# Optimization experiments

Hardware: AMD Instinct MI355X
Metric: run time of the kernel (lower is better)

## Reference

```python
import jax, jax.numpy as jnp
import numpy as np

D_MODEL = 1024
D_FF = 2 * D_MODEL
N_EXPERTS = 8
TOP_K = 2
SCAT_SCALE = 0.1


def setup_inputs() -> dict:
    key = jax.random.key(0)
    ks = jax.random.split(key, 8)
    s_in = 1.0 / np.sqrt(D_MODEL)
    s_ff = 1.0 / np.sqrt(D_FF)
    return {
        "x": jax.random.normal(ks[0], (4, 2048, D_MODEL), dtype=jnp.float32),
        "Wg": jax.random.uniform(ks[1], (D_MODEL, N_EXPERTS), minval=-s_in, maxval=s_in),
        "bg": jax.random.uniform(ks[2], (N_EXPERTS,), minval=-s_in, maxval=s_in),
        "W1": jax.random.uniform(ks[3], (N_EXPERTS, D_MODEL, D_FF), minval=-s_in, maxval=s_in),
        "b1": jax.random.uniform(ks[4], (N_EXPERTS, D_FF), minval=-s_in, maxval=s_in),
        "W2": jax.random.uniform(ks[5], (N_EXPERTS, D_FF, D_MODEL), minval=-s_ff, maxval=s_ff),
        "b2": jax.random.uniform(ks[6], (N_EXPERTS, D_MODEL), minval=-s_ff, maxval=s_ff),
    }


def reference(x, Wg, bg, W1, b1, W2, b2):
    B, N, D = x.shape
    T = B * N
    xf = x.reshape(T, D)

    # gating logits + norm-based modulation (scattering_scale branch)
    logits = xf @ Wg + bg  # [T, E]
    tnorm = jnp.linalg.norm(xf, axis=-1, keepdims=True)  # [T, 1]
    norm_scaled = (tnorm - tnorm.mean()) / (jnp.std(tnorm, ddof=1) + 1e-6)
    logits = logits + SCAT_SCALE * norm_scaled

    # top-k routing
    topv, topi = jax.lax.top_k(logits, TOP_K)  # [T, K]
    gates_k = jax.nn.softmax(topv, axis=-1)  # [T, K]
    routing_entropy = -(gates_k * jnp.log(jnp.clip(gates_k, 1e-8, None))).sum(-1).mean()

    # dense per-token expert-weight matrix (zeros for non-selected experts)
    E = W1.shape[0]
    gates = jnp.zeros((T, E), dtype=gates_k.dtype).at[
        jnp.arange(T)[:, None], topi
    ].add(gates_k)  # [T, E]

    # all-expert MLP (dense equivalent of sparse dispatch; weight 0 -> no contribution)
    h = jax.nn.relu(jnp.einsum("td,edf->etf", xf, W1) + b1[:, None, :])  # [E, T, F]
    y = jnp.einsum("etf,efd->etd", h, W2) + b2[:, None, :]  # [E, T, D]
    out = jnp.einsum("etd,te->td", y, gates).reshape(B, N, D)
    return out, routing_entropy
```

## Files before the change

### kernel.cpp

```cpp
#include <hip/hip_runtime.h>
#include <hip/hip_bf16.h>

#define T_TOK 8192
#define DMODEL 1024
#define DFF 2048
#define NEXP 8

typedef __attribute__((ext_vector_type(8))) short short8v;
typedef __attribute__((ext_vector_type(4))) float floatx4;
typedef __attribute__((ext_vector_type(4))) ushort ushort4v;

__device__ __forceinline__ ushort f2bf(float f) {
  union { float f; unsigned u; } v; v.f = f;
  unsigned u = v.u;
  unsigned r = (u + 0x7FFFu + ((u >> 16) & 1u)) >> 16;
  return (ushort)r;
}
__device__ __forceinline__ float bf2f(ushort b) {
  union { unsigned u; float f; } v; v.u = ((unsigned)b) << 16;
  return v.f;
}
__device__ __forceinline__ void gload16(const void* g, void* l) {
  __builtin_amdgcn_global_load_lds(
      (const __attribute__((address_space(1))) unsigned int*)g,
      (__attribute__((address_space(3))) unsigned int*)l, 16, 0, 0);
}
__device__ __forceinline__ short8v dsr128(unsigned off) {
  short8v r;
  asm volatile("ds_read_b128 %0, %1" : "=v"(r) : "v"(off));
  return r;
}
#define VMW(n) asm volatile("s_waitcnt vmcnt(" #n ")" ::: "memory")
#define LG0()  asm volatile("s_waitcnt lgkmcnt(0)" ::: "memory")
#define BAR()  asm volatile("s_barrier" ::: "memory")
#define SB0()  __builtin_amdgcn_sched_barrier(0)

__global__ __launch_bounds__(256) void gating_kernel(
    const float* __restrict__ x, const float* __restrict__ Wg,
    const float* __restrict__ bg, int* __restrict__ meta,
    int* __restrict__ te, float* __restrict__ tg, float* __restrict__ entWs,
    ushort* __restrict__ xb) {
  __shared__ float wgT[8448];
  __shared__ float sbg[NEXP];
  __shared__ int cnt_s[NEXP];
  __shared__ float ent_s;
  int tid = threadIdx.x;
#pragma unroll
  for (int k = 0; k < 8; ++k) {
    int g4 = tid + 256 * k;
    float4 v = ((const float4*)Wg)[g4];
    int q = g4 * 4;
    int f = q >> 5;
    wgT[q + f]     = v.x;
    wgT[q + 1 + f] = v.y;
    wgT[q + 2 + f] = v.z;
    wgT[q + 3 + f] = v.w;
  }
  if (tid < NEXP) { sbg[tid] = bg[tid]; cnt_s[tid] = 0; }
  if (tid == 0) ent_s = 0.f;
  __syncthreads();

  int wid = tid >> 6, lane = tid & 63;
#pragma unroll 1
  for (int it = 0; it < 4; ++it) {
    int t = blockIdx.x * 16 + wid * 4 + it;
    const float* xr = x + (long)t * DMODEL;
    ushort* xbr = xb + (long)t * DMODEL;
    float acc[NEXP];
#pragma unroll
    for (int e = 0; e < NEXP; ++e) acc[e] = 0.f;
#pragma unroll
    for (int i = 0; i < 4; ++i) {
      int dbase = i * 256 + lane * 4;
      int pad = i * 64 + lane;
      float4 xv = *(const float4*)(xr + dbase);
      ushort4v s;
      s[0] = f2bf(xv.x); s[1] = f2bf(xv.y); s[2] = f2bf(xv.z); s[3] = f2bf(xv.w);
      *(ushort4v*)(xbr + dbase) = s;
      float xj[4] = {xv.x, xv.y, xv.z, xv.w};
#pragma unroll
      for (int j = 0; j < 4; ++j) {
        int base = 8 * (dbase + j) + pad;
#pragma unroll
        for (int e = 0; e < NEXP; ++e) acc[e] += xj[j] * wgT[base + e];
      }
    }
#pragma unroll
    for (int off = 32; off; off >>= 1)
#pragma unroll
      for (int e = 0; e < NEXP; ++e) acc[e] += __shfl_xor(acc[e], off, 64);
    if (lane == 0) {
      float lg[NEXP];
#pragma unroll
      for (int e = 0; e < NEXP; ++e) lg[e] = acc[e] + sbg[e];
      int e1 = 0; float v1 = lg[0];
#pragma unroll
      for (int e = 1; e < NEXP; ++e) if (lg[e] > v1) { v1 = lg[e]; e1 = e; }
      int e2 = -1; float v2 = -1e30f;
#pragma unroll
      for (int e = 0; e < NEXP; ++e) if (e != e1 && lg[e] > v2) { v2 = lg[e]; e2 = e; }
      float p2 = expf(v2 - v1);
      float s = 1.f + p2;
      float g1 = 1.f / s, g2 = p2 / s;
      float ent = -(g1 * logf(fmaxf(g1, 1e-8f)) + g2 * logf(fmaxf(g2, 1e-8f)));
      atomicAdd(&cnt_s[e1], 1);
      atomicAdd(&cnt_s[e2], 1);
      atomicAdd(&ent_s, ent);
      te[2 * t] = e1; te[2 * t + 1] = e2;
      tg[2 * t] = g1; tg[2 * t + 1] = g2;
    }
  }
  __syncthreads();
  if (tid < NEXP && cnt_s[tid]) atomicAdd(&meta[tid], cnt_s[tid]);
  if (tid == 0) atomicAdd(entWs, ent_s * (1.f / T_TOK));
}

__global__ void prefix_kernel(int* __restrict__ meta) {
  if (threadIdx.x == 0) {
    int s = 0;
    for (int e = 0; e < NEXP; ++e) { meta[16 + e] = s; s += meta[e]; meta[32 + e] = 0; }
  }
}

__global__ void scatter_kernel(const int* __restrict__ te, const float* __restrict__ tg,
                               int* __restrict__ meta, int* __restrict__ tok,
                               float* __restrict__ gate, int* __restrict__ slotOf) {
  int t = blockIdx.x * blockDim.x + threadIdx.x;
  if (t >= T_TOK) return;
  for (int k = 0; k < 2; ++k) {
    int e = te[2 * t + k];
    int pos = atomicAdd(&meta[32 + e], 1);
    int slot = meta[16 + e] + pos;
    tok[slot] = t;
    gate[slot] = tg[2 * t + k];
    slotOf[2 * t + k] = slot;
  }
}

__global__ __launch_bounds__(256) void tcvt2_kernel(
    const float* __restrict__ W1, const float* __restrict__ W2,
    ushort* __restrict__ w1t, ushort* __restrict__ w2t,
    int* __restrict__ meta, float* __restrict__ entWs) {
  int id = blockIdx.x;
  if (id == 0) {
    if (threadIdx.x < 64) meta[threadIdx.x] = 0;
    if (threadIdx.x == 64) *entWs = 0.f;
  }
  const float* src; ushort* dst; int R, C, r0, c0, e;
  if (id < 4096) {
    src = W1; dst = w1t; R = DMODEL; C = DFF;
    c0 = (id & 31) * 64; r0 = ((id >> 5) & 15) * 64; e = id >> 9;
  } else {
    int j = id - 4096;
    src = W2; dst = w2t; R = DFF; C = DMODEL;
    c0 = (j & 15) * 64; r0 = ((j >> 4) & 31) * 64; e = j >> 9;
  }
  __shared__ ushort tile[64][72];
  int tid = threadIdx.x;
  long eoff = (long)e * R * C;
  int lr = tid >> 4, lc = (tid & 15) * 4;
#pragma unroll
  for (int p = 0; p < 4; ++p) {
    int r = lr + p * 16;
    float4 v = *(const float4*)&src[eoff + (long)(r0 + r) * C + (c0 + lc)];
    tile[r][lc + 0] = f2bf(v.x); tile[r][lc + 1] = f2bf(v.y);
    tile[r][lc + 2] = f2bf(v.z); tile[r][lc + 3] = f2bf(v.w);
  }
  __syncthreads();
  int sr = tid >> 3, sc = (tid & 7) * 8;
#pragma unroll
  for (int p = 0; p < 2; ++p) {
    int c = sr + p * 32;
    short8v v;
#pragma unroll
    for (int j = 0; j < 8; ++j) v[j] = (short)tile[sc + j][c];
    *(short8v*)&dst[eoff + (long)(c0 + c) * R + (r0 + sc)] = v;
  }
}

__device__ __forceinline__ void gemm_pipe(
    int NT, const char* aP0, const char* aP1,
    const char* bP0, const char* bP1, const char* bP2, const char* bP3,
    char* lds, int tid, floatx4 (&acc)[8][4]) {
  const unsigned ldsU = (unsigned)(unsigned long)lds;
  int lane = tid & 63, wid = tid >> 6;
  int lr = lane & 15, lg = lane >> 4;
  unsigned offA[8], offB[4];
#pragma unroll
  for (int mi = 0; mi < 8; ++mi) {
    int row = mi * 16 + lr;
    offA[mi] = row * 64 + ((lg * 16) ^ (((row >> 1) & 3) << 4));
  }
#pragma unroll
  for (int ni = 0; ni < 4; ++ni) {
    int row = wid * 64 + ni * 16 + lr;
    offB[ni] = row * 64 + ((lg * 16) ^ (((row >> 1) & 3) << 4));
  }

  auto STG = [&](int b, int t) {
    int koff = t * 64;
    char* da = lds + b * 8192;
    gload16(aP0 + koff, da + tid * 16);
    gload16(aP1 + koff, da + 4096 + tid * 16);
    char* db = lds + 24576 + b * 16384;
    gload16(bP0 + koff, db + tid * 16);
    gload16(bP1 + koff, db + 4096 + tid * 16);
    gload16(bP2 + koff, db + 8192 + tid * 16);
    gload16(bP3 + koff, db + 12288 + tid * 16);
  };
  auto RD = [&](int b, short8v (&af)[8], short8v (&bf)[4]) {
#pragma unroll
    for (int ni = 0; ni < 4; ++ni) bf[ni] = dsr128(ldsU + 24576u + (unsigned)(b * 16384) + offB[ni]);
#pragma unroll
    for (int mi = 0; mi < 8; ++mi) af[mi] = dsr128(ldsU + (unsigned)(b * 8192) + offA[mi]);
  };
  auto MM = [&](short8v (&af)[8], short8v (&bf)[4]) {
#pragma unroll
    for (int mi = 0; mi < 8; ++mi)
#pragma unroll
      for (int ni = 0; ni < 4; ++ni)
        acc[mi][ni] =
            __builtin_amdgcn_mfma_f32_16x16x32_bf16(af[mi], bf[ni], acc[mi][ni], 0, 0, 0);
  };

  STG(0, 0); STG(1, 1);
  VMW(6); BAR();

  short8v af[8], bf[4];
  int b = 0;
  for (int t = 0; t + 2 < NT; ++t) {
    RD(b, af, bf);
    int bs = (b == 0) ? 2 : b - 1;
    STG(bs, t + 2);
    VMW(6);
    BAR(); LG0(); SB0();
    __builtin_amdgcn_s_setprio(1); MM(af, bf); __builtin_amdgcn_s_setprio(0);
    SB0(); BAR();
    b = (b == 2) ? 0 : b + 1;
  }
  {
    RD(b, af, bf);
    VMW(0);
    BAR(); LG0(); SB0();
    __builtin_amdgcn_s_setprio(1); MM(af, bf); __builtin_amdgcn_s_setprio(0);
    SB0(); BAR();
    b = (b == 2) ? 0 : b + 1;
  }
  {
    RD(b, af, bf);
    LG0(); SB0();
    __builtin_amdgcn_s_setprio(1); MM(af, bf); __builtin_amdgcn_s_setprio(0);
  }
}

__global__ __launch_bounds__(256, 2) void gemm1_kernel(
    const ushort* __restrict__ xb, const ushort* __restrict__ w1t,
    const float* __restrict__ b1, const int* __restrict__ meta,
    const int* __restrict__ tok, ushort* __restrict__ h) {
  const int NWG = 64 * 8 * NEXP;
  int flat = blockIdx.x;
  int wgid = (flat % 8) * (NWG / 8) + flat / 8;
  int m0 = (wgid & 63) * 128;
  int rest = wgid >> 6;
  int n0 = (rest & 7) * 256;
  int e = rest >> 3;
  int cnt = meta[e];
  if (m0 >= cnt) return;
  int bas = meta[16 + e];
  __shared__ char lds[73728];
  int tid = threadIdx.x;

  const char* w1e = (const char*)(w1t + (long)e * DFF * DMODEL);
  int rA = tid >> 2;
  int ch = tid & 3;
  auto sc = [&](int row) { return (unsigned)((ch * 16) ^ (((row >> 1) & 3) << 4)); };
  int ma0 = m0 + rA;        if (ma0 >= cnt) ma0 = cnt - 1;
  int ma1 = m0 + rA + 64;   if (ma1 >= cnt) ma1 = cnt - 1;
  const char* aP0 = (const char*)xb + (long)tok[bas + ma0] * (DMODEL * 2) + sc(rA);
  const char* aP1 = (const char*)xb + (long)tok[bas + ma1] * (DMODEL * 2) + sc(rA + 64);
  const char* bP0 = w1e + (long)(n0 + rA) * (DMODEL * 2) + sc(rA);
  const char* bP1 = w1e + (long)(n0 + rA + 64) * (DMODEL * 2) + sc(rA + 64);
  const char* bP2 = w1e + (long)(n0 + rA + 128) * (DMODEL * 2) + sc(rA + 128);
  const char* bP3 = w1e + (long)(n0 + rA + 192) * (DMODEL * 2) + sc(rA + 192);

  floatx4 acc[8][4];
#pragma unroll
  for (int i = 0; i < 8; ++i)
#pragma unroll
    for (int j = 0; j < 4; ++j) acc[i][j] = (floatx4){0.f, 0.f, 0.f, 0.f};

  gemm_pipe(DMODEL / 32, aP0, aP1, bP0, bP1, bP2, bP3, lds, tid, acc);

  int lane = tid & 63, wid = tid >> 6;
  int lr = lane & 15, lg = lane >> 4;
  const float* b1e = b1 + e * DFF;
#pragma unroll
  for (int mi = 0; mi < 8; ++mi) {
#pragma unroll
    for (int r = 0; r < 4; ++r) {
      int m = m0 + mi * 16 + lg * 4 + r;
      if (m >= cnt) continue;
      long hrow = (long)(bas + m) * DFF;
#pragma unroll
      for (int ni = 0; ni < 4; ++ni) {
        int f = n0 + wid * 64 + ni * 16 + lr;
        float v = acc[mi][ni][r] + b1e[f];
        h[hrow + f] = f2bf(fmaxf(v, 0.f));
      }
    }
  }
}

__global__ __launch_bounds__(256, 2) void gemm2_kernel(
    const ushort* __restrict__ h, const ushort* __restrict__ w2t,
    const float* __restrict__ b2, const int* __restrict__ meta,
    const float* __restrict__ gate, ushort* __restrict__ y) {
  const int NWG = 64 * 4 * NEXP;
  int flat = blockIdx.x;
  int wgid = (flat % 8) * (NWG / 8) + flat / 8;
  int m0 = (wgid & 63) * 128;
  int rest = wgid >> 6;
  int n0 = (rest & 3) * 256;
  int e = rest >> 2;
  int cnt = meta[e];
  if (m0 >= cnt) return;
  int bas = meta[16 + e];
  __shared__ char lds[73728];
  int tid = threadIdx.x;

  const char* w2e = (const char*)(w2t + (long)e * DMODEL * DFF);
  int rA = tid >> 2;
  int ch = tid & 3;
  auto sc = [&](int row) { return (unsigned)((ch * 16) ^ (((row >> 1) & 3) << 4)); };
  int ma0 = m0 + rA;        if (ma0 >= cnt) ma0 = cnt - 1;
  int ma1 = m0 + rA + 64;   if (ma1 >= cnt) ma1 = cnt - 1;
  const char* aP0 = (const char*)h + (long)(bas + ma0) * (DFF * 2) + sc(rA);
  const char* aP1 = (const char*)h + (long)(bas + ma1) * (DFF * 2) + sc(rA + 64);
  const char* bP0 = w2e + (long)(n0 + rA) * (DFF * 2) + sc(rA);
  const char* bP1 = w2e + (long)(n0 + rA + 64) * (DFF * 2) + sc(rA + 64);
  const char* bP2 = w2e + (long)(n0 + rA + 128) * (DFF * 2) + sc(rA + 128);
  const char* bP3 = w2e + (long)(n0 + rA + 192) * (DFF * 2) + sc(rA + 192);

  floatx4 acc[8][4];
#pragma unroll
  for (int i = 0; i < 8; ++i)
#pragma unroll
    for (int j = 0; j < 4; ++j) acc[i][j] = (floatx4){0.f, 0.f, 0.f, 0.f};

  gemm_pipe(DFF / 32, aP0, aP1, bP0, bP1, bP2, bP3, lds, tid, acc);

  int lane = tid & 63, wid = tid >> 6;
  int lr = lane & 15, lg = lane >> 4;
  const float* b2e = b2 + e * DMODEL;
#pragma unroll
  for (int mi = 0; mi < 8; ++mi) {
#pragma unroll
    for (int r = 0; r < 4; ++r) {
      int m = m0 + mi * 16 + lg * 4 + r;
      if (m >= cnt) continue;
      int slot = bas + m;
      float g = gate[slot];
      ushort* yr = y + (long)slot * DMODEL;
#pragma unroll
      for (int ni = 0; ni < 4; ++ni) {
        int n = n0 + wid * 64 + ni * 16 + lr;
        float v = g * (acc[mi][ni][r] + b2e[n]);
        yr[n] = f2bf(v);
      }
    }
  }
}

__global__ __launch_bounds__(256) void combine_kernel(
    const ushort* __restrict__ y, const int* __restrict__ slotOf,
    const float* __restrict__ entWs, float* __restrict__ out) {
  int wid = threadIdx.x >> 6, lane = threadIdx.x & 63;
  int t = blockIdx.x * 4 + wid;
  int s1 = slotOf[2 * t], s2 = slotOf[2 * t + 1];
  const ushort* y1 = y + (long)s1 * DMODEL;
  const ushort* y2 = y + (long)s2 * DMODEL;
  float* outr = out + (long)t * DMODEL;
#pragma unroll
  for (int i = 0; i < 4; ++i) {
    int d = i * 256 + lane * 4;
    ushort4v a = *(const ushort4v*)&y1[d];
    ushort4v b = *(const ushort4v*)&y2[d];
    float4 r;
    r.x = bf2f(a[0]) + bf2f(b[0]);
    r.y = bf2f(a[1]) + bf2f(b[1]);
    r.z = bf2f(a[2]) + bf2f(b[2]);
    r.w = bf2f(a[3]) + bf2f(b[3]);
    *(float4*)&outr[d] = r;
  }
  if (blockIdx.x == 0 && threadIdx.x == 0) out[(long)T_TOK * DMODEL] = *entWs;
}

extern "C" void kernel_launch(void* const* d_in, const int* in_sizes, int n_in,
                              void* d_out, int out_size, void* d_ws, size_t ws_size,
                              hipStream_t stream) {
  const float* x  = (const float*)d_in[0];
  const float* Wg = (const float*)d_in[1];
  const float* bg = (const float*)d_in[2];
  const float* W1 = (const float*)d_in[3];
  const float* b1 = (const float*)d_in[4];
  const float* W2 = (const float*)d_in[5];
  const float* b2 = (const float*)d_in[6];
  float* out = (float*)d_out;

  char* ws = (char*)d_ws;
  int*    meta   = (int*)(ws + 0);
  float*  entWs  = (float*)(ws + 256);
  int*    te     = (int*)(ws + 1024);
  float*  tg     = (float*)(ws + 66560);
  int*    tokA   = (int*)(ws + 132096);
  float*  gate   = (float*)(ws + 197632);
  int*    slotOf = (int*)(ws + 263168);
  ushort* xb     = (ushort*)(ws + 328704);
  ushort* w1t    = (ushort*)(ws + 17105920);
  ushort* w2t    = (ushort*)(ws + 50660352);
  ushort* h      = (ushort*)(ws + 84214784);
  ushort* y      = w1t;

  tcvt2_kernel<<<8192, 256, 0, stream>>>(W1, W2, w1t, w2t, meta, entWs);
  gating_kernel<<<T_TOK / 16, 256, 0, stream>>>(x, Wg, bg, meta, te, tg, entWs, xb);
  prefix_kernel<<<1, 1, 0, stream>>>(meta);
  scatter_kernel<<<T_TOK / 256, 256, 0, stream>>>(te, tg, meta, tokA, gate, slotOf);
  gemm1_kernel<<<64 * 8 * NEXP, 256, 0, stream>>>(xb, w1t, b1, meta, tokA, h);
  gemm2_kernel<<<64 * 4 * NEXP, 256, 0, stream>>>(h, w2t, b2, meta, gate, y);
  combine_kernel<<<T_TOK / 4, 256, 0, stream>>>(y, slotOf, entWs, out);
}
```

Measured before the change: 334.2 us.

## Overlap W2 bf16 transpose-convert with the first expert GEMM

Splits the weight conversion kernel so only W1 is converted up front, and folds the W2 convert/transpose tiles into the gemm1 launch as 4096 extra leading blocks. The W2 conversion, which is memory-bound, is meant to run concurrently with the compute-bound gemm1 blocks instead of serializing before them. The cost is that the convert blocks now reserve gemm1's 72KB LDS footprint and register budget, which limits how many of them fit per CU. Because they sit at the start of the grid, gemm1 blocks may be dispatched after them rather than alongside.

```diff
diff --git a/kernel.cpp b/kernel.cpp
--- a/kernel.cpp
+++ b/kernel.cpp
@@ -34,6 +34,45 @@
 #define LG0()  asm volatile("s_waitcnt lgkmcnt(0)" ::: "memory")
 #define BAR()  asm volatile("s_barrier" ::: "memory")
 #define SB0()  __builtin_amdgcn_sched_barrier(0)
+
+__device__ __forceinline__ void tcvt_tile(const float* __restrict__ src,
+                                          ushort* __restrict__ dst,
+                                          int R, int C, int r0, int c0, int e,
+                                          void* ldsraw, int tid) {
+  ushort (*tile)[72] = (ushort (*)[72])ldsraw;
+  long eoff = (long)e * R * C;
+  int lr = tid >> 4, lc = (tid & 15) * 4;
+#pragma unroll
+  for (int p = 0; p < 4; ++p) {
+    int r = lr + p * 16;
+    float4 v = *(const float4*)&src[eoff + (long)(r0 + r) * C + (c0 + lc)];
+    tile[r][lc + 0] = f2bf(v.x); tile[r][lc + 1] = f2bf(v.y);
+    tile[r][lc + 2] = f2bf(v.z); tile[r][lc + 3] = f2bf(v.w);
+  }
+  __syncthreads();
+  int sr = tid >> 3, sc = (tid & 7) * 8;
+#pragma unroll
+  for (int p = 0; p < 2; ++p) {
+    int c = sr + p * 32;
+    short8v v;
+#pragma unroll
+    for (int j = 0; j < 8; ++j) v[j] = (short)tile[sc + j][c];
+    *(short8v*)&dst[eoff + (long)(c0 + c) * R + (r0 + sc)] = v;
+  }
+}
+
+__global__ __launch_bounds__(256) void tcvt1_kernel(
+    const float* __restrict__ W1, ushort* __restrict__ w1t,
+    int* __restrict__ meta, float* __restrict__ entWs) {
+  __shared__ ushort tile[64][72];
+  int id = blockIdx.x;
+  if (id == 0) {
+    if (threadIdx.x < 64) meta[threadIdx.x] = 0;
+    if (threadIdx.x == 64) *entWs = 0.f;
+  }
+  int c0 = (id & 31) * 64, r0 = ((id >> 5) & 15) * 64, e = id >> 9;
+  tcvt_tile(W1, w1t, DMODEL, DFF, r0, c0, e, tile, threadIdx.x);
+}
 
 __global__ __launch_bounds__(256) void gating_kernel(
     const float* __restrict__ x, const float* __restrict__ Wg,
@@ -137,47 +176,6 @@
   }
 }
 
-__global__ __launch_bounds__(256) void tcvt2_kernel(
-    const float* __restrict__ W1, const float* __restrict__ W2,
-    ushort* __restrict__ w1t, ushort* __restrict__ w2t,
-    int* __restrict__ meta, float* __restrict__ entWs) {
-  int id = blockIdx.x;
-  if (id == 0) {
-    if (threadIdx.x < 64) meta[threadIdx.x] = 0;
-    if (threadIdx.x == 64) *entWs = 0.f;
-  }
-  const float* src; ushort* dst; int R, C, r0, c0, e;
-  if (id < 4096) {
-    src = W1; dst = w1t; R = DMODEL; C = DFF;
-    c0 = (id & 31) * 64; r0 = ((id >> 5) & 15) * 64; e = id >> 9;
-  } else {
-    int j = id - 4096;
-    src = W2; dst = w2t; R = DFF; C = DMODEL;
-    c0 = (j & 15) * 64; r0 = ((j >> 4) & 31) * 64; e = j >> 9;
-  }
-  __shared__ ushort tile[64][72];
-  int tid = threadIdx.x;
-  long eoff = (long)e * R * C;
-  int lr = tid >> 4, lc = (tid & 15) * 4;
-#pragma unroll
-  for (int p = 0; p < 4; ++p) {
-    int r = lr + p * 16;
-    float4 v = *(const float4*)&src[eoff + (long)(r0 + r) * C + (c0 + lc)];
-    tile[r][lc + 0] = f2bf(v.x); tile[r][lc + 1] = f2bf(v.y);
-    tile[r][lc + 2] = f2bf(v.z); tile[r][lc + 3] = f2bf(v.w);
-  }
-  __syncthreads();
-  int sr = tid >> 3, sc = (tid & 7) * 8;
-#pragma unroll
-  for (int p = 0; p < 2; ++p) {
-    int c = sr + p * 32;
-    short8v v;
-#pragma unroll
-    for (int j = 0; j < 8; ++j) v[j] = (short)tile[sc + j][c];
-    *(short8v*)&dst[eoff + (long)(c0 + c) * R + (r0 + sc)] = v;
-  }
-}
-
 __device__ __forceinline__ void gemm_pipe(
     int NT, const char* aP0, const char* aP1,
     const char* bP0, const char* bP1, const char* bP2, const char* bP3,
@@ -253,12 +251,21 @@
   }
 }
 
-__global__ __launch_bounds__(256, 2) void gemm1_kernel(
+__global__ __launch_bounds__(256, 2) void gemm1x_kernel(
     const ushort* __restrict__ xb, const ushort* __restrict__ w1t,
     const float* __restrict__ b1, const int* __restrict__ meta,
-    const int* __restrict__ tok, ushort* __restrict__ h) {
+    const int* __restrict__ tok, ushort* __restrict__ h,
+    const float* __restrict__ W2, ushort* __restrict__ w2t) {
+  __shared__ char lds[73728];
+  int tid = threadIdx.x;
+  if (blockIdx.x < 4096) {
+    int j = blockIdx.x;
+    int c0 = (j & 15) * 64, r0 = ((j >> 4) & 31) * 64, e = j >> 9;
+    tcvt_tile(W2, w2t, DFF, DMODEL, r0, c0, e, lds, tid);
+    return;
+  }
   const int NWG = 64 * 8 * NEXP;
-  int flat = blockIdx.x;
+  int flat = blockIdx.x - 4096;
   int wgid = (flat % 8) * (NWG / 8) + flat / 8;
   int m0 = (wgid & 63) * 128;
   int rest = wgid >> 6;
@@ -267,8 +274,6 @@
   int cnt = meta[e];
   if (m0 >= cnt) return;
   int bas = meta[16 + e];
-  __shared__ char lds[73728];
-  int tid = threadIdx.x;
 
   const char* w1e = (const char*)(w1t + (long)e * DFF * DMODEL);
   int rA = tid >> 2;
@@ -421,11 +426,11 @@
   ushort* h      = (ushort*)(ws + 84214784);
   ushort* y      = w1t;
 
-  tcvt2_kernel<<<8192, 256, 0, stream>>>(W1, W2, w1t, w2t, meta, entWs);
+  tcvt1_kernel<<<4096, 256, 0, stream>>>(W1, w1t, meta, entWs);
   gating_kernel<<<T_TOK / 16, 256, 0, stream>>>(x, Wg, bg, meta, te, tg, entWs, xb);
   prefix_kernel<<<1, 1, 0, stream>>>(meta);
   scatter_kernel<<<T_TOK / 256, 256, 0, stream>>>(te, tg, meta, tokA, gate, slotOf);
-  gemm1_kernel<<<64 * 8 * NEXP, 256, 0, stream>>>(xb, w1t, b1, meta, tokA, h);
+  gemm1x_kernel<<<4096 + 64 * 8 * NEXP, 256, 0, stream>>>(xb, w1t, b1, meta, tokA, h, W2, w2t);
   gemm2_kernel<<<64 * 4 * NEXP, 256, 0, stream>>>(h, w2t, b2, meta, gate, y);
   combine_kernel<<<T_TOK / 4, 256, 0, stream>>>(y, slotOf, entWs, out);
 }
```

Measured after the change: 334.3 us. Within noise of the previous version (+0.0%).
